# Kernel tuning notes

Measured on AMD Instinct MI355X. Metric: run time of the kernel, lower is better.

Reference implementation:

```python
import jax, jax.numpy as jnp
import numpy as np

NUM_GRAPHS = 1024


def setup_inputs() -> dict:
    key = jax.random.key(0)
    k1, k2, k3, k4 = jax.random.split(key, 4)
    N, D, H = 500000, 256, 256
    x = jax.random.normal(k1, (N, D), dtype=jnp.float32)
    batch = jnp.sort(jax.random.randint(k2, (N,), 0, NUM_GRAPHS, dtype=jnp.int64))
    # Linear init scale ~ 1/sqrt(fan_in)
    W1 = jax.random.normal(k3, (D, H), dtype=jnp.float32) / np.sqrt(D)
    b1 = jnp.zeros((H,), dtype=jnp.float32)
    W2 = jax.random.normal(k4, (H, 1), dtype=jnp.float32) / np.sqrt(H)
    b2 = jnp.zeros((1,), dtype=jnp.float32)
    return {"x": x, "batch": batch, "W1": W1, "b1": b1, "W2": W2, "b2": b2}


def reference(x, batch, W1, b1, W2, b2):
    # Two-layer attention MLP -> scores [N, 1] (dropout = identity at eval)
    scores = jnp.tanh(x @ W1 + b1) @ W2 + b2
    # Softmax over dim 0 (global over all nodes, as in the source)
    attn = jax.nn.softmax(scores, axis=0)  # [N, 1]
    # Weighted scatter-add pooling per graph id
    pooled = jax.ops.segment_sum(x * attn, batch, num_segments=NUM_GRAPHS)
    return pooled  # [NUM_GRAPHS, D]
```

## Files before the change

### kernel.cpp

```cpp
#include <hip/hip_runtime.h>
#include <stdint.h>

#define NBLOCKS 256
#define TROWS 64
#define B_FRAGS 127
#define XT_OFF (B_FRAGS * 1024)
#define SPART_OFF (XT_OFF + TROWS * 512)
#define SMEM_BYTES (SPART_OFF + 512)

typedef __attribute__((ext_vector_type(8))) short bfrag_t;
typedef __attribute__((ext_vector_type(4))) float f32x4;
typedef __attribute__((ext_vector_type(2))) unsigned int u32x2;

static __device__ __forceinline__ unsigned short f2bf(float f) {
  unsigned int u = __float_as_uint(f);
  u += 0x7fffu + ((u >> 16) & 1u);
  return (unsigned short)(u >> 16);
}

static __device__ __forceinline__ float tanh_fast(float s) {
  float e = __builtin_exp2f(s * 2.8853900817779268f);
  float r = __builtin_amdgcn_rcpf(1.f + e);
  return __builtin_fmaf(-2.f, r, 1.f);
}

static __device__ __forceinline__ float readlane_f(float v, int l) {
  return __uint_as_float(__builtin_amdgcn_readlane(__float_as_uint(v), l));
}

static __device__ __forceinline__ bfrag_t pack8(f32x4 a, f32x4 b) {
  union { bfrag_t v; unsigned int u[4]; } r;
  asm("v_cvt_pk_bf16_f32 %0, %1, %2" : "=v"(r.u[0]) : "v"(a[0]), "v"(a[1]));
  asm("v_cvt_pk_bf16_f32 %0, %1, %2" : "=v"(r.u[1]) : "v"(a[2]), "v"(a[3]));
  asm("v_cvt_pk_bf16_f32 %0, %1, %2" : "=v"(r.u[2]) : "v"(b[0]), "v"(b[1]));
  asm("v_cvt_pk_bf16_f32 %0, %1, %2" : "=v"(r.u[3]) : "v"(b[2]), "v"(b[3]));
  return r.v;
}

#define GLD16(gp, lp) __builtin_amdgcn_global_load_lds( \
    (const __attribute__((address_space(1))) void*)(gp), \
    (__attribute__((address_space(3))) void*)(lp), 16, 0, 0)

__global__ void prep_w1_kernel(const float* __restrict__ W1, unsigned short* __restrict__ W1f) {
  const int bx = blockIdx.x;
  const int l = threadIdx.x;
  const int cc = bx >> 3, kk = bx & 7;
  const int h = cc * 16 + (l & 15);
  const int kbase = kk * 32 + ((l >> 4) << 3);
  bfrag_t pk;
#pragma unroll
  for (int j = 0; j < 8; ++j) pk[j] = (short)f2bf(W1[(size_t)(kbase + j) * 256 + h]);
  *(bfrag_t*)(W1f + (size_t)(bx * 64 + l) * 8) = pk;
}

__attribute__((amdgpu_flat_work_group_size(512, 512), amdgpu_waves_per_eu(2, 2)))
__global__ void attnpool_kernel(const float* __restrict__ x,
                                const int* __restrict__ batch,
                                const unsigned short* __restrict__ W1f,
                                const float* __restrict__ b1,
                                const float* __restrict__ W2,
                                const float* __restrict__ b2,
                                float* __restrict__ out,
                                float* __restrict__ Zp,
                                int N, int base, int rem) {
  extern __shared__ char smem[];
  char* Bl = smem;
  char* xt = smem + XT_OFF;
  float* spart = (float*)(smem + SPART_OFF);

  const int t = threadIdx.x;
  const int lane = t & 63;
  const int wv = t >> 6;
  const int rg = wv & 3;
  const int cg = wv >> 2;
  const int l15 = lane & 15;
  const int hi = lane >> 4;

  const int blk = blockIdx.x;
  const int cnt = base + (blk < rem ? 1 : 0);
  const int tile0 = blk * base + min(blk, rem);

#pragma unroll
  for (int i = 0; i < 16; ++i) {
    const int f = wv * 16 + i;
    if (f < B_FRAGS) GLD16(W1f + (size_t)f * 512 + lane * 8, Bl + f * 1024);
  }

  float b1v[8], w2v[8];
#pragma unroll
  for (int i = 0; i < 8; ++i) {
    b1v[i] = b1[(cg * 8 + i) * 16 + l15];
    w2v[i] = W2[(cg * 8 + i) * 16 + l15];
  }
  const float b2c = b2[0];

  const int srow = t >> 5;
  const int soct = t & 31;
  f32x4 sreg[8];
  auto issue_loads = [&](int tile) {
#pragma unroll
    for (int p = 0; p < 4; ++p) {
      const int row = p * 16 + srow;
      const int rgb = min(tile * TROWS + row, N - 1);
      const float* s = x + (size_t)rgb * 256 + soct * 8;
      sreg[2 * p] = *(const f32x4*)s;
      sreg[2 * p + 1] = *(const f32x4*)(s + 4);
    }
  };
  auto write_tile = [&]() {
#pragma unroll
    for (int p = 0; p < 4; ++p) {
      const int row = p * 16 + srow;
      *(bfrag_t*)(xt + row * 512 + ((soct * 16) ^ ((row & 7) << 4))) =
          pack8(sreg[2 * p], sreg[2 * p + 1]);
    }
  };

  issue_loads(tile0);
  write_tile();
  __syncthreads();

  float zacc = 0.f;
  f32x4 pacc = {0.f, 0.f, 0.f, 0.f};
  int gcur = -1;

  auto flush = [&]() {
    float* po = out + (size_t)gcur * 256 + lane * 4;
    atomicAdd(po + 0, pacc[0]); atomicAdd(po + 1, pacc[1]);
    atomicAdd(po + 2, pacc[2]); atomicAdd(po + 3, pacc[3]);
    pacc[0] = pacc[1] = pacc[2] = pacc[3] = 0.f;
  };

  for (int tt = 0; tt < cnt; ++tt) {
    const int tile = tile0 + tt;
    const int R0 = tile * TROWS;

    if (tt + 1 < cnt) issue_loads(tile + 1);

    bfrag_t A0[8];
    {
      const int arow = rg * 16 + l15;
      const int sw = (l15 & 7) << 4;
      const char* ap = xt + arow * 512;
#pragma unroll
      for (int kk = 0; kk < 8; ++kk)
        A0[kk] = *(const bfrag_t*)(ap + ((kk * 64 + hi * 16) ^ sw));
    }

    float s0v[4] = {0.f, 0.f, 0.f, 0.f};
#pragma unroll
    for (int i = 0; i < 8; ++i) {
      const int cc = cg * 8 + i;
      f32x4 acc = {0.f, 0.f, 0.f, 0.f};
#pragma unroll
      for (int kk = 0; kk < 8; ++kk) {
        const int frag = cc * 8 + kk;
        bfrag_t Bk;
        if (frag == B_FRAGS)
          Bk = *(const bfrag_t*)(W1f + (size_t)frag * 512 + lane * 8);
        else
          Bk = *(const bfrag_t*)(Bl + frag * 1024 + lane * 16);
        acc = __builtin_amdgcn_mfma_f32_16x16x32_bf16(A0[kk], Bk, acc, 0, 0, 0);
      }
#pragma unroll
      for (int r = 0; r < 4; ++r)
        s0v[r] += tanh_fast(acc[r] + b1v[i]) * w2v[i];
    }

#pragma unroll
    for (int r = 0; r < 4; ++r) {
      float v = s0v[r];
      v += __shfl_xor(v, 1); v += __shfl_xor(v, 2);
      v += __shfl_xor(v, 4); v += __shfl_xor(v, 8);
      s0v[r] = v;
    }
    if (l15 == 0) {
#pragma unroll
      for (int r = 0; r < 4; ++r)
        spart[cg * 64 + rg * 16 + hi * 4 + r] = s0v[r];
    }
    __syncthreads();

    f32x4 w0v;
#pragma unroll
    for (int r = 0; r < 4; ++r) {
      const int row = rg * 16 + hi * 4 + r;
      const float s = s0v[r] + spart[(cg ^ 1) * 64 + row] + b2c;
      w0v[r] = (R0 + row < N) ? __expf(s) : 0.f;
    }
    if (cg == 0) {
      float z = w0v[0] + w0v[1] + w0v[2] + w0v[3];
      z += __shfl_xor(z, 16);
      z += __shfl_xor(z, 32);
      zacc += z;
    }

    float wlane;
    {
      const int rq = lane & 3;
      const float ca = (rq == 0) ? w0v[0] : w0v[1];
      const float cb = (rq == 2) ? w0v[2] : w0v[3];
      const float c = (rq < 2) ? ca : cb;
      const int srcl = (((lane >> 2) & 3) << 4) + rq;
      wlane = __shfl(c, srcl);
    }

    int bid = batch[min(R0 + rg * 16 + l15, N - 1)];

    const int g_first = __builtin_amdgcn_readlane(bid, cg * 8);
    const int g_last = __builtin_amdgcn_readlane(bid, cg * 8 + 7);
    if (g_first != gcur) { if (gcur >= 0) flush(); gcur = g_first; }
    const int rowb = rg * 16 + cg * 8;
    if (g_first == g_last) {
#pragma unroll
      for (int r = 0; r < 8; ++r) {
        const float wr = readlane_f(wlane, cg * 8 + r);
        const int row = rowb + r;
        const u32x2 v = *(const u32x2*)(xt + row * 512 + ((lane * 8) ^ ((row & 7) << 4)));
        pacc[0] = __builtin_fmaf(wr, __uint_as_float(v[0] << 16), pacc[0]);
        pacc[1] = __builtin_fmaf(wr, __uint_as_float(v[0] & 0xffff0000u), pacc[1]);
        pacc[2] = __builtin_fmaf(wr, __uint_as_float(v[1] << 16), pacc[2]);
        pacc[3] = __builtin_fmaf(wr, __uint_as_float(v[1] & 0xffff0000u), pacc[3]);
      }
    } else {
      for (int r = 0; r < 8; ++r) {
        const int g = __builtin_amdgcn_readlane(bid, cg * 8 + r);
        if (g != gcur) { flush(); gcur = g; }
        const float wr = readlane_f(wlane, cg * 8 + r);
        const int row = rowb + r;
        const u32x2 v = *(const u32x2*)(xt + row * 512 + ((lane * 8) ^ ((row & 7) << 4)));
        pacc[0] = __builtin_fmaf(wr, __uint_as_float(v[0] << 16), pacc[0]);
        pacc[1] = __builtin_fmaf(wr, __uint_as_float(v[0] & 0xffff0000u), pacc[1]);
        pacc[2] = __builtin_fmaf(wr, __uint_as_float(v[1] << 16), pacc[2]);
        pacc[3] = __builtin_fmaf(wr, __uint_as_float(v[1] & 0xffff0000u), pacc[3]);
      }
    }

    __syncthreads();
    if (tt + 1 < cnt) write_tile();
    __syncthreads();
  }

  if (gcur >= 0) flush();
  if (lane == 0 && zacc != 0.f) atomicAdd(Zp, zacc);
}

__global__ void finalize_kernel(float* __restrict__ out, const float* __restrict__ Zp, int n4) {
  const int i = blockIdx.x * blockDim.x + threadIdx.x;
  if (i < n4) {
    const float zi = 1.f / Zp[0];
    f32x4* p = (f32x4*)out;
    f32x4 v = p[i];
    v[0] *= zi; v[1] *= zi; v[2] *= zi; v[3] *= zi;
    p[i] = v;
  }
}

extern "C" void kernel_launch(void* const* d_in, const int* in_sizes, int n_in,
                              void* d_out, int out_size, void* d_ws, size_t ws_size,
                              hipStream_t stream) {
  const float* x  = (const float*)d_in[0];
  const int* batch = (const int*)d_in[1];
  const float* W1 = (const float*)d_in[2];
  const float* b1 = (const float*)d_in[3];
  const float* W2 = (const float*)d_in[4];
  const float* b2 = (const float*)d_in[5];
  float* out = (float*)d_out;
  const int N = in_sizes[1];

  unsigned short* W1f = (unsigned short*)d_ws;
  float* Zp = (float*)((char*)d_ws + 131072);

  static int attr_done = 0;
  if (!attr_done) {
    hipFuncSetAttribute((const void*)attnpool_kernel,
                        hipFuncAttributeMaxDynamicSharedMemorySize, SMEM_BYTES);
    attr_done = 1;
  }

  const int ntiles = (N + TROWS - 1) / TROWS;
  const int base = ntiles / NBLOCKS;
  const int rem = ntiles % NBLOCKS;

  hipMemsetAsync(d_out, 0, (size_t)out_size * sizeof(float), stream);
  hipMemsetAsync(Zp, 0, sizeof(float), stream);
  prep_w1_kernel<<<128, 64, 0, stream>>>(W1, W1f);
  attnpool_kernel<<<NBLOCKS, 512, SMEM_BYTES, stream>>>(x, batch, W1f, b1, W2, b2,
                                                        out, Zp, N, base, rem);
  finalize_kernel<<<(out_size / 4 + 255) / 256, 256, 0, stream>>>(out, Zp, out_size / 4);
}
```

Measured before the change: 178.9 us.

## Double-buffer x tile register prefetch two tiles ahead with lighter barriers

Prefetches x rows two tiles ahead into alternating register buffers (sA/sB), so global loads have a full extra tile iteration to land before they are packed into LDS. The loop is unrolled by two to swap buffers statically. __syncthreads is replaced with a barrier that waits only on lgkmcnt, so the barrier no longer waits on outstanding global (vmcnt) loads. This costs 32 extra VGPRs of staging registers under a 2-waves-per-EU occupancy constraint, which risks spills.

Result: no change. 175.5 us (-1.9%).

```diff
diff --git a/kernel.cpp b/kernel.cpp
--- a/kernel.cpp
+++ b/kernel.cpp
@@ -40,6 +40,11 @@
 #define GLD16(gp, lp) __builtin_amdgcn_global_load_lds( \
     (const __attribute__((address_space(1))) void*)(gp), \
     (__attribute__((address_space(3))) void*)(lp), 16, 0, 0)
+
+#define BAR_LGKM() do { \
+  asm volatile("s_waitcnt lgkmcnt(0)" ::: "memory"); \
+  __builtin_amdgcn_s_barrier(); \
+  asm volatile("" ::: "memory"); } while (0)
 
 __global__ void prep_w1_kernel(const float* __restrict__ W1, unsigned short* __restrict__ W1f) {
   const int bx = blockIdx.x;
@@ -96,8 +101,8 @@
 
   const int srow = t >> 5;
   const int soct = t & 31;
-  f32x4 sreg[8];
-  auto issue_loads = [&](int tile) {
+  f32x4 sA[8], sB[8];
+  auto issue_loads = [&](int tile, f32x4 (&sreg)[8]) {
 #pragma unroll
     for (int p = 0; p < 4; ++p) {
       const int row = p * 16 + srow;
@@ -107,7 +112,7 @@
       sreg[2 * p + 1] = *(const f32x4*)(s + 4);
     }
   };
-  auto write_tile = [&]() {
+  auto write_tile = [&](f32x4 (&sreg)[8]) {
 #pragma unroll
     for (int p = 0; p < 4; ++p) {
       const int row = p * 16 + srow;
@@ -115,10 +120,6 @@
           pack8(sreg[2 * p], sreg[2 * p + 1]);
     }
   };
-
-  issue_loads(tile0);
-  write_tile();
-  __syncthreads();
 
   float zacc = 0.f;
   f32x4 pacc = {0.f, 0.f, 0.f, 0.f};
@@ -131,11 +132,11 @@
     pacc[0] = pacc[1] = pacc[2] = pacc[3] = 0.f;
   };
 
-  for (int tt = 0; tt < cnt; ++tt) {
+  auto body = [&](int tt, f32x4 (&sIss)[8], f32x4 (&sWr)[8]) {
     const int tile = tile0 + tt;
     const int R0 = tile * TROWS;
 
-    if (tt + 1 < cnt) issue_loads(tile + 1);
+    if (tt + 2 < cnt) issue_loads(tile + 2, sIss);
 
     bfrag_t A0[8];
     {
@@ -179,7 +180,7 @@
       for (int r = 0; r < 4; ++r)
         spart[cg * 64 + rg * 16 + hi * 4 + r] = s0v[r];
     }
-    __syncthreads();
+    BAR_LGKM();
 
     f32x4 w0v;
 #pragma unroll
@@ -236,9 +237,22 @@
       }
     }
 
-    __syncthreads();
-    if (tt + 1 < cnt) write_tile();
-    __syncthreads();
+    BAR_LGKM();
+    if (tt + 1 < cnt) write_tile(sWr);
+    BAR_LGKM();
+  };
+
+  issue_loads(tile0, sA);
+  write_tile(sA);
+  if (cnt > 1) issue_loads(tile0 + 1, sB);
+  BAR_LGKM();
+
+  int tt = 0;
+  for (;;) {
+    body(tt, sA, sB);
+    if (++tt >= cnt) break;
+    body(tt, sB, sA);
+    if (++tt >= cnt) break;
   }
 
   if (gcur >= 0) flush();
```

## Double-buffer x tile, split waves 2x4 for A reuse, cut barriers

Applied to the files above, without the earlier changes.

The kernel now keeps two LDS buffers for the bf16 x tile, so the next tile is written into the spare buffer and one barrier per iteration goes away. Waves are regrouped into 2 row groups by 4 column groups, so each wave computes 32 rows by 64 columns and reuses each B fragment for two MFMAs. This lowers LDS reads of W1 per MFMA. The softmax weight reduction is reorganised across the four column-group partials in spart. To fit both buffers, fewer W1 fragments stay resident in LDS (94 instead of 127), so more B fragments are read from global memory each tile, which adds global traffic.

New measurement: 279.0 us. 1.56x slower.

```diff
diff --git a/kernel.cpp b/kernel.cpp
--- a/kernel.cpp
+++ b/kernel.cpp
@@ -3,10 +3,11 @@
 
 #define NBLOCKS 256
 #define TROWS 64
-#define B_FRAGS 127
-#define XT_OFF (B_FRAGS * 1024)
-#define SPART_OFF (XT_OFF + TROWS * 512)
-#define SMEM_BYTES (SPART_OFF + 512)
+#define B_FRAGS 94
+#define XT0_OFF (B_FRAGS * 1024)
+#define XT1_OFF (XT0_OFF + 32768)
+#define SPART_OFF (XT1_OFF + 32768)
+#define SMEM_BYTES (SPART_OFF + 1024)
 
 typedef __attribute__((ext_vector_type(8))) short bfrag_t;
 typedef __attribute__((ext_vector_type(4))) float f32x4;
@@ -40,6 +41,11 @@
 #define GLD16(gp, lp) __builtin_amdgcn_global_load_lds( \
     (const __attribute__((address_space(1))) void*)(gp), \
     (__attribute__((address_space(3))) void*)(lp), 16, 0, 0)
+
+#define BAR_LGKM() do { \
+  asm volatile("s_waitcnt lgkmcnt(0)" ::: "memory"); \
+  __builtin_amdgcn_s_barrier(); \
+  asm volatile("" ::: "memory"); } while (0)
 
 __global__ void prep_w1_kernel(const float* __restrict__ W1, unsigned short* __restrict__ W1f) {
   const int bx = blockIdx.x;
@@ -65,14 +71,13 @@
                                 int N, int base, int rem) {
   extern __shared__ char smem[];
   char* Bl = smem;
-  char* xt = smem + XT_OFF;
   float* spart = (float*)(smem + SPART_OFF);
 
   const int t = threadIdx.x;
   const int lane = t & 63;
   const int wv = t >> 6;
-  const int rg = wv & 3;
-  const int cg = wv >> 2;
+  const int rg = wv & 1;
+  const int cgr = wv >> 1;
   const int l15 = lane & 15;
   const int hi = lane >> 4;
 
@@ -81,16 +86,16 @@
   const int tile0 = blk * base + min(blk, rem);
 
 #pragma unroll
-  for (int i = 0; i < 16; ++i) {
-    const int f = wv * 16 + i;
+  for (int i = 0; i < 12; ++i) {
+    const int f = wv * 12 + i;
     if (f < B_FRAGS) GLD16(W1f + (size_t)f * 512 + lane * 8, Bl + f * 1024);
   }
 
-  float b1v[8], w2v[8];
-#pragma unroll
-  for (int i = 0; i < 8; ++i) {
-    b1v[i] = b1[(cg * 8 + i) * 16 + l15];
-    w2v[i] = W2[(cg * 8 + i) * 16 + l15];
+  float b1v[4], w2v[4];
+#pragma unroll
+  for (int c = 0; c < 4; ++c) {
+    b1v[c] = b1[(cgr * 4 + c) * 16 + l15];
+    w2v[c] = W2[(cgr * 4 + c) * 16 + l15];
   }
   const float b2c = b2[0];
 
@@ -107,18 +112,14 @@
       sreg[2 * p + 1] = *(const f32x4*)(s + 4);
     }
   };
-  auto write_tile = [&]() {
+  auto write_tile = [&](char* buf) {
 #pragma unroll
     for (int p = 0; p < 4; ++p) {
       const int row = p * 16 + srow;
-      *(bfrag_t*)(xt + row * 512 + ((soct * 16) ^ ((row & 7) << 4))) =
+      *(bfrag_t*)(buf + row * 512 + ((soct * 16) ^ ((row & 7) << 4))) =
           pack8(sreg[2 * p], sreg[2 * p + 1]);
     }
   };
-
-  issue_loads(tile0);
-  write_tile();
-  __syncthreads();
 
   float zacc = 0.f;
   f32x4 pacc = {0.f, 0.f, 0.f, 0.f};
@@ -131,92 +132,92 @@
     pacc[0] = pacc[1] = pacc[2] = pacc[3] = 0.f;
   };
 
+  issue_loads(tile0);
+  write_tile(smem + XT0_OFF);
+  BAR_LGKM();
+
   for (int tt = 0; tt < cnt; ++tt) {
     const int tile = tile0 + tt;
     const int R0 = tile * TROWS;
+    char* xc = smem + ((tt & 1) ? XT1_OFF : XT0_OFF);
+    char* xn = smem + ((tt & 1) ? XT0_OFF : XT1_OFF);
 
     if (tt + 1 < cnt) issue_loads(tile + 1);
 
-    bfrag_t A0[8];
-    {
-      const int arow = rg * 16 + l15;
-      const int sw = (l15 & 7) << 4;
-      const char* ap = xt + arow * 512;
-#pragma unroll
-      for (int kk = 0; kk < 8; ++kk)
-        A0[kk] = *(const bfrag_t*)(ap + ((kk * 64 + hi * 16) ^ sw));
+    f32x4 acc[4][2] = {};
+    const int arow0 = rg * 32 + l15;
+    const int sw = (l15 & 7) << 4;
+#pragma unroll
+    for (int kk = 0; kk < 8; ++kk) {
+      const int co = (kk * 64 + hi * 16) ^ sw;
+      const bfrag_t A0 = *(const bfrag_t*)(xc + arow0 * 512 + co);
+      const bfrag_t A1 = *(const bfrag_t*)(xc + (arow0 + 16) * 512 + co);
+#pragma unroll
+      for (int c = 0; c < 4; ++c) {
+        const int frag = (cgr * 4 + c) * 8 + kk;
+        bfrag_t Bk;
+        if (frag < B_FRAGS)
+          Bk = *(const bfrag_t*)(Bl + frag * 1024 + lane * 16);
+        else
+          Bk = *(const bfrag_t*)(W1f + (size_t)frag * 512 + lane * 8);
+        acc[c][0] = __builtin_amdgcn_mfma_f32_16x16x32_bf16(A0, Bk, acc[c][0], 0, 0, 0);
+        acc[c][1] = __builtin_amdgcn_mfma_f32_16x16x32_bf16(A1, Bk, acc[c][1], 0, 0, 0);
+      }
     }
 
     float s0v[4] = {0.f, 0.f, 0.f, 0.f};
-#pragma unroll
-    for (int i = 0; i < 8; ++i) {
-      const int cc = cg * 8 + i;
-      f32x4 acc = {0.f, 0.f, 0.f, 0.f};
-#pragma unroll
-      for (int kk = 0; kk < 8; ++kk) {
-        const int frag = cc * 8 + kk;
-        bfrag_t Bk;
-        if (frag == B_FRAGS)
-          Bk = *(const bfrag_t*)(W1f + (size_t)frag * 512 + lane * 8);
-        else
-          Bk = *(const bfrag_t*)(Bl + frag * 1024 + lane * 16);
-        acc = __builtin_amdgcn_mfma_f32_16x16x32_bf16(A0[kk], Bk, acc, 0, 0, 0);
-      }
-#pragma unroll
-      for (int r = 0; r < 4; ++r)
-        s0v[r] += tanh_fast(acc[r] + b1v[i]) * w2v[i];
-    }
-
+    float s1v[4] = {0.f, 0.f, 0.f, 0.f};
+#pragma unroll
+    for (int c = 0; c < 4; ++c)
+#pragma unroll
+      for (int r = 0; r < 4; ++r) {
+        s0v[r] += tanh_fast(acc[c][0][r] + b1v[c]) * w2v[c];
+        s1v[r] += tanh_fast(acc[c][1][r] + b1v[c]) * w2v[c];
+      }
 #pragma unroll
     for (int r = 0; r < 4; ++r) {
-      float v = s0v[r];
-      v += __shfl_xor(v, 1); v += __shfl_xor(v, 2);
-      v += __shfl_xor(v, 4); v += __shfl_xor(v, 8);
-      s0v[r] = v;
+      float v0 = s0v[r], v1 = s1v[r];
+      v0 += __shfl_xor(v0, 1); v0 += __shfl_xor(v0, 2);
+      v0 += __shfl_xor(v0, 4); v0 += __shfl_xor(v0, 8);
+      v1 += __shfl_xor(v1, 1); v1 += __shfl_xor(v1, 2);
+      v1 += __shfl_xor(v1, 4); v1 += __shfl_xor(v1, 8);
+      s0v[r] = v0; s1v[r] = v1;
     }
     if (l15 == 0) {
 #pragma unroll
-      for (int r = 0; r < 4; ++r)
-        spart[cg * 64 + rg * 16 + hi * 4 + r] = s0v[r];
-    }
-    __syncthreads();
-
-    f32x4 w0v;
-#pragma unroll
-    for (int r = 0; r < 4; ++r) {
-      const int row = rg * 16 + hi * 4 + r;
-      const float s = s0v[r] + spart[(cg ^ 1) * 64 + row] + b2c;
-      w0v[r] = (R0 + row < N) ? __expf(s) : 0.f;
-    }
-    if (cg == 0) {
-      float z = w0v[0] + w0v[1] + w0v[2] + w0v[3];
-      z += __shfl_xor(z, 16);
-      z += __shfl_xor(z, 32);
-      zacc += z;
-    }
-
+      for (int r = 0; r < 4; ++r) {
+        spart[cgr * 64 + rg * 32 + hi * 4 + r] = s0v[r];
+        spart[cgr * 64 + rg * 32 + 16 + hi * 4 + r] = s1v[r];
+      }
+    }
+    BAR_LGKM();
+
+    const int prow = wv * 8 + (lane & 7);
     float wlane;
     {
-      const int rq = lane & 3;
-      const float ca = (rq == 0) ? w0v[0] : w0v[1];
-      const float cb = (rq == 2) ? w0v[2] : w0v[3];
-      const float c = (rq < 2) ? ca : cb;
-      const int srcl = (((lane >> 2) & 3) << 4) + rq;
-      wlane = __shfl(c, srcl);
-    }
-
-    int bid = batch[min(R0 + rg * 16 + l15, N - 1)];
-
-    const int g_first = __builtin_amdgcn_readlane(bid, cg * 8);
-    const int g_last = __builtin_amdgcn_readlane(bid, cg * 8 + 7);
+      float v = spart[((lane >> 3) & 3) * 64 + prow];
+      v += __shfl_xor(v, 8);
+      v += __shfl_xor(v, 16);
+      wlane = (R0 + prow < N) ? __expf(v + b2c) : 0.f;
+    }
+    {
+      float zv = (lane < 8) ? wlane : 0.f;
+      zv += __shfl_xor(zv, 1);  zv += __shfl_xor(zv, 2);  zv += __shfl_xor(zv, 4);
+      zv += __shfl_xor(zv, 8);  zv += __shfl_xor(zv, 16); zv += __shfl_xor(zv, 32);
+      zacc += zv;
+    }
+    int bid = batch[min(R0 + prow, N - 1)];
+
+    const int g_first = __builtin_amdgcn_readlane(bid, 0);
+    const int g_last = __builtin_amdgcn_readlane(bid, 7);
     if (g_first != gcur) { if (gcur >= 0) flush(); gcur = g_first; }
-    const int rowb = rg * 16 + cg * 8;
+    const int rowb = wv * 8;
     if (g_first == g_last) {
 #pragma unroll
       for (int r = 0; r < 8; ++r) {
-        const float wr = readlane_f(wlane, cg * 8 + r);
+        const float wr = readlane_f(wlane, r);
         const int row = rowb + r;
-        const u32x2 v = *(const u32x2*)(xt + row * 512 + ((lane * 8) ^ ((row & 7) << 4)));
+        const u32x2 v = *(const u32x2*)(xc + row * 512 + ((lane * 8) ^ ((row & 7) << 4)));
         pacc[0] = __builtin_fmaf(wr, __uint_as_float(v[0] << 16), pacc[0]);
         pacc[1] = __builtin_fmaf(wr, __uint_as_float(v[0] & 0xffff0000u), pacc[1]);
         pacc[2] = __builtin_fmaf(wr, __uint_as_float(v[1] << 16), pacc[2]);
@@ -224,11 +225,11 @@
       }
     } else {
       for (int r = 0; r < 8; ++r) {
-        const int g = __builtin_amdgcn_readlane(bid, cg * 8 + r);
+        const int g = __builtin_amdgcn_readlane(bid, r);
         if (g != gcur) { flush(); gcur = g; }
-        const float wr = readlane_f(wlane, cg * 8 + r);
+        const float wr = readlane_f(wlane, r);
         const int row = rowb + r;
-        const u32x2 v = *(const u32x2*)(xt + row * 512 + ((lane * 8) ^ ((row & 7) << 4)));
+        const u32x2 v = *(const u32x2*)(xc + row * 512 + ((lane * 8) ^ ((row & 7) << 4)));
         pacc[0] = __builtin_fmaf(wr, __uint_as_float(v[0] << 16), pacc[0]);
         pacc[1] = __builtin_fmaf(wr, __uint_as_float(v[0] & 0xffff0000u), pacc[1]);
         pacc[2] = __builtin_fmaf(wr, __uint_as_float(v[1] << 16), pacc[2]);
@@ -236,9 +237,8 @@
       }
     }
 
-    __syncthreads();
-    if (tt + 1 < cnt) write_tile();
-    __syncthreads();
+    if (tt + 1 < cnt) write_tile(xn);
+    BAR_LGKM();
   }
 
   if (gcur >= 0) flush();
```
